# Kernel tuning notes

Hardware: AMD Instinct MI355X
Metric: run time of the kernel (lower is better)

Reference implementation:

```python
import jax, jax.numpy as jnp
import numpy as np

KS = 5          # kernel_size per pseudo-dim
DIM = 2         # pseudo-coordinate dims
KTOT = KS ** DIM  # 25 spline kernel slots
N_NODES = 50000
N_EDGES = 1600000
N_GRAPHS = 64
F_IN, H1, H2, N_CLS = 32, 32, 64, 10


def spline_basis(edge_attr):
    """Open B-spline basis, degree 1, dim=2, kernel_size=5.
    Returns basis [E,4] and flat kernel indices [E,4]."""
    v = edge_attr * (KS - 1)                    # [E,2] in [0, KS-1]
    lo = jnp.floor(v)
    frac = v - lo                               # [E,2]
    lo_i = lo.astype(jnp.int32)
    # per-dim basis values for offsets s in {0,1}: (1-frac), frac
    bas_d = jnp.stack([1.0 - frac, frac], axis=-1)            # [E,2,2]
    idx_d = jnp.minimum(lo_i[..., None] + jnp.arange(2, dtype=jnp.int32), KS - 1)  # [E,2,2]
    basis = bas_d[:, 0, :, None] * bas_d[:, 1, None, :]       # [E,2,2]
    kidx = idx_d[:, 0, :, None] + KS * idx_d[:, 1, None, :]   # [E,2,2]
    E = edge_attr.shape[0]
    return basis.reshape(E, 4), kidx.reshape(E, 4)


def spline_conv(x, src, dst, basis, kidx, W, Wroot, b):
    """SplineConv: gather x[src], spline-weight, scatter-mean to dst, + root + bias.
    W: [KTOT, Cin, Cout]."""
    N, Cin = x.shape
    x_j = x[src]                                # [E, Cin] gather
    # accumulate per-(node, kernel-slot) weighted sums; loop over 4 nonzero combos
    T = jnp.zeros((N * KTOT, Cin), dtype=x.dtype)
    for s in range(4):
        seg = dst * KTOT + kidx[:, s]
        T = T + jax.ops.segment_sum(basis[:, s, None] * x_j, seg,
                                    num_segments=N * KTOT)
    T = T.reshape(N, KTOT, Cin)
    out = jnp.einsum('nki,kio->no', T, W)       # [N, Cout]
    deg = jax.ops.segment_sum(jnp.ones_like(dst, dtype=x.dtype), dst,
                              num_segments=N)
    out = out / jnp.maximum(deg, 1.0)[:, None]  # aggr='mean'
    return out + x @ Wroot + b


def global_mean_pool(x, batch, num_graphs):
    s = jax.ops.segment_sum(x, batch, num_segments=num_graphs)
    cnt = jax.ops.segment_sum(jnp.ones((x.shape[0],), x.dtype), batch,
                              num_segments=num_graphs)
    return s / jnp.maximum(cnt, 1.0)[:, None]


def setup_inputs() -> dict:
    key = jax.random.key(0)
    ks = jax.random.split(key, 16)
    x = jax.random.normal(ks[0], (N_NODES, F_IN), jnp.float32)
    edge_index = jax.random.randint(ks[1], (2, N_EDGES), 0, N_NODES, jnp.int32)
    edge_attr = jax.random.uniform(ks[2], (N_EDGES, DIM), jnp.float32)
    batch = jnp.sort(jax.random.randint(ks[3], (N_NODES,), 0, N_GRAPHS, jnp.int32))

    def w(k, shape, fan_in):
        return jax.random.normal(k, shape, jnp.float32) / np.sqrt(fan_in)

    return {
        'x': x, 'edge_index': edge_index, 'edge_attr': edge_attr, 'batch': batch,
        'W1': w(ks[4], (KTOT, F_IN, H1), F_IN), 'root1': w(ks[5], (F_IN, H1), F_IN),
        'b1': jnp.zeros((H1,), jnp.float32),
        'W2': w(ks[6], (KTOT, H1, H2), H1), 'root2': w(ks[7], (H1, H2), H1),
        'b2': jnp.zeros((H2,), jnp.float32),
        'lin1_w': w(ks[8], (H2, 64), H2), 'lin1_b': jnp.zeros((64,), jnp.float32),
        'lin2_w': w(ks[9], (64, 64), 64), 'lin2_b': jnp.zeros((64,), jnp.float32),
        'lin3_w': w(ks[10], (64, N_CLS), 64), 'lin3_b': jnp.zeros((N_CLS,), jnp.float32),
    }


def reference(x, edge_index, edge_attr, batch, W1, root1, b1, W2, root2, b2,
              lin1_w, lin1_b, lin2_w, lin2_b, lin3_w, lin3_b):
    src, dst = edge_index[0], edge_index[1]
    basis, kidx = spline_basis(edge_attr)
    h = jax.nn.relu(spline_conv(x, src, dst, basis, kidx, W1, root1, b1))
    h = jax.nn.relu(spline_conv(h, src, dst, basis, kidx, W2, root2, b2))
    g = global_mean_pool(h, batch, N_GRAPHS)                # [B, 64]
    g = g * jax.nn.sigmoid(g @ lin1_w + lin1_b)
    g = g * jax.nn.sigmoid(g @ lin2_w + lin2_b)
    return jax.nn.log_softmax(g @ lin3_w + lin3_b, axis=1)  # [B, N_CLS]
```

## Files before the change

kernel.cpp:

```cpp
#include <hip/hip_runtime.h>
#include <hip/hip_bf16.h>
#include <hip/hip_fp16.h>
#include <cstdint>


typedef _Float16 half8 __attribute__((ext_vector_type(8)));
typedef float f32x4 __attribute__((ext_vector_type(4)));

__device__ __forceinline__ int lowb(const int* __restrict__ a, int n, int v) {
  int lo = 0, hi = n;
  while (lo < hi) { int m = (lo + hi) >> 1; if (a[m] < v) lo = m + 1; else hi = m; }
  return lo;
}

__global__ void hist_kernel(const int* __restrict__ dst, int E, int* __restrict__ deg) {
  int e = blockIdx.x * 256 + threadIdx.x;
  if (e < E) atomicAdd(&deg[dst[e]], 1);
}

__global__ __launch_bounds__(1024) void scan_block_kernel(
    const int* __restrict__ deg, int n, int* __restrict__ offs, int* __restrict__ bsums) {
  __shared__ int wsum[16];
  int t = threadIdx.x;
  int gi = blockIdx.x * 1024 + t;
  int v = (gi < n) ? deg[gi] : 0;
  int lane = t & 63, w = t >> 6;
  int x = v;
  #pragma unroll
  for (int d = 1; d < 64; d <<= 1) { int y = __shfl_up(x, d, 64); if (lane >= d) x += y; }
  if (lane == 63) wsum[w] = x;
  __syncthreads();
  if (w == 0) {
    int s = (lane < 16) ? wsum[lane] : 0;
    #pragma unroll
    for (int d = 1; d < 16; d <<= 1) { int y = __shfl_up(s, d, 64); if (lane >= d) s += y; }
    if (lane < 16) wsum[lane] = s;
  }
  __syncthreads();
  int add = (w > 0) ? wsum[w - 1] : 0;
  x += add;
  if (gi < n) offs[gi + 1] = x;
  if (t == 1023) bsums[blockIdx.x] = x;
}

__global__ __launch_bounds__(64) void scan_bsums_kernel(
    const int* __restrict__ bsums, int nb, int* __restrict__ boff) {
  int l = threadIdx.x;
  int v = (l < nb) ? bsums[l] : 0;
  int x = v;
  #pragma unroll
  for (int d = 1; d < 64; d <<= 1) { int y = __shfl_up(x, d, 64); if (l >= d) x += y; }
  if (l < nb) boff[l] = x - v;
}

__global__ void scan_add_kernel(int* __restrict__ offs, const int* __restrict__ boff, int n) {
  int i = blockIdx.x * 256 + threadIdx.x;
  if (i < n) offs[i + 1] += boff[i >> 10];
  if (i == 0) offs[0] = 0;
}

__global__ void scatter_kernel(const int* __restrict__ src, const int* __restrict__ dst,
                               const float2* __restrict__ attr, int E,
                               const int* __restrict__ offs, int* __restrict__ cursor,
                               int2* __restrict__ emeta) {
  int e = blockIdx.x * 256 + threadIdx.x;
  if (e < E) {
    float2 a = attr[e];
    float v0 = a.x * 4.f, v1 = a.y * 4.f;
    int i00 = min((int)v0, 3);
    int i10 = min((int)v1, 3);
    float f0 = v0 - (float)i00;
    float f1 = v1 - (float)i10;
    int f0q = (int)(f0 * 4095.f + 0.5f);
    int f1q = (int)(f1 * 4095.f + 0.5f);
    int yw = (i10 * 5 + i00) | (i10 << 5) | (f0q << 7) | (f1q << 19);
    int d = dst[e];
    int p = offs[d] + atomicAdd(&cursor[d], 1);
    emeta[p] = make_int2(src[e], yw);
  }
}

__global__ void x2h_kernel(const float* __restrict__ X, __half* __restrict__ Xh, int n) {
  int i = blockIdx.x * 256 + threadIdx.x;
  if (i < n) Xh[i] = __float2half(X[i]);
}

__global__ void w2h_kernel(const float* __restrict__ W, __half* __restrict__ Wh,
                           int ncolTot, int COUT) {
  int idx = blockIdx.x * 256 + threadIdx.x;
  if (idx < ncolTot * 32) {
    int col = idx >> 5, i = idx & 31;
    int kk = col / COUT, ch = col - kk * COUT;
    Wh[idx] = __float2half(W[(kk * 32 + i) * COUT + ch]);
  }
}

__global__ __launch_bounds__(256) void mfma_ygemm(
    const __half* __restrict__ Xh, const __half* __restrict__ Wh,
    __half* __restrict__ Y, int N, int ncol, int strideY) {
  __shared__ __half Ls[16 * 264];
  const int t = threadIdx.x;
  const int w = t >> 6, lane = t & 63;
  const int rowBase = blockIdx.x * 16;
  const int colBase = blockIdx.y * 256;
  const int kOff = (lane >> 4) * 8;
  int arow = min(rowBase + (lane & 15), N - 1);
  const half8 Af = *(const half8*)(Xh + (size_t)arow * 32 + kOff);
  half8 Bf[4];
  #pragma unroll
  for (int c = 0; c < 4; ++c) {
    int col = min(colBase + w * 64 + c * 16 + (lane & 15), ncol - 1);
    Bf[c] = *(const half8*)(Wh + (size_t)col * 32 + kOff);
  }
  f32x4 zero = {0.f, 0.f, 0.f, 0.f};
  f32x4 acc[4];
  #pragma unroll
  for (int c = 0; c < 4; ++c)
    acc[c] = __builtin_amdgcn_mfma_f32_16x16x32_f16(Af, Bf[c], zero, 0, 0, 0);
  #pragma unroll
  for (int c = 0; c < 4; ++c) {
    int col = w * 64 + c * 16 + (lane & 15);
    int r0 = (lane >> 4) * 4;
    #pragma unroll
    for (int r = 0; r < 4; ++r)
      Ls[(r0 + r) * 264 + col] = __float2half(acc[c][r]);
  }
  __syncthreads();
  int row = rowBase + (t >> 4);
  int cseg = (t & 15) * 16;
  if (row < N && colBase + cseg < ncol) {
    int4* dst = (int4*)(Y + (size_t)row * (size_t)strideY + colBase + cseg);
    const int4* srcp = (const int4*)(Ls + (t >> 4) * 264 + cseg);
    dst[0] = srcp[0];
    dst[1] = srcp[1];
  }
}

template <int COUT>
__global__ __launch_bounds__(256) void gather_kernel(
    const int2* __restrict__ emeta, const int* __restrict__ offs,
    const __half* __restrict__ Y, int strideY,
    float* __restrict__ hagg, int N, int g0, int g1, int first, int fused,
    const __half* __restrict__ X, const float* __restrict__ root,
    const float* __restrict__ bias, __half* __restrict__ hout) {
  __shared__ float Rs[32 * COUT];
  const int t = threadIdx.x;
  if (fused) {
    #pragma unroll
    for (int q = 0; q < (8 * COUT) / 256; ++q)
      *(float4*)&Rs[(t + q * 256) * 4] = *(const float4*)&root[(t + q * 256) * 4];
    __syncthreads();
  }
  const int w = t >> 6, lane = t & 63;
  const int n = blockIdx.x * 4 + w;
  if (n >= N) return;
  const int q4 = lane >> 4, r = lane & 15;
  const int di0 = q4 & 1, di1 = q4 >> 1;
  constexpr int CPL = COUT / 16;
  const int kBias = di0 + 5 * di1 - 5 * g0;
  const int laneCh = r * CPL;
  float acc[CPL];
  #pragma unroll
  for (int j = 0; j < CPL; ++j) acc[j] = 0.f;
  const int beg = offs[n], end = offs[n + 1];
  for (int b0 = beg; b0 < end; b0 += 64) {
    const int cnt = min(64, end - b0);
    int2 m = emeta[b0 + min(lane, cnt - 1)];
    int myS = m.x, myY = m.y;
    for (int j0 = 0; j0 < cnt; j0 += 4) {
      float wg[4];
      __half2 yv[4][CPL / 2];
      #pragma unroll
      for (int u = 0; u < 4; ++u) {
        int j = j0 + u;
        int jc = (j < cnt) ? j : 0;
        int s  = __builtin_amdgcn_readlane(myS, jc);
        int yw = __builtin_amdgcn_readlane(myY, jc);
        int k0 = yw & 31;
        int i10 = (yw >> 5) & 3;
        float f0 = (float)((yw >> 7) & 4095) * (1.f / 4095.f);
        float f1 = (float)((yw >> 19) & 4095) * (1.f / 4095.f);
        float wt = (di0 ? f0 : 1.f - f0) * (di1 ? f1 : 1.f - f1);
        bool skip = (j >= cnt) || (i10 < g0) || (i10 >= g1);
        wg[u] = skip ? 0.f : wt;
        int rowL = skip ? 0 : (k0 + kBias);
        const __half2* yp =
            (const __half2*)(Y + (size_t)s * (size_t)strideY + rowL * COUT + laneCh);
        #pragma unroll
        for (int p = 0; p < CPL / 2; ++p) yv[u][p] = yp[p];
      }
      #pragma unroll
      for (int u = 0; u < 4; ++u)
        #pragma unroll
        for (int p = 0; p < CPL / 2; ++p) {
          float2 f = __half22float2(yv[u][p]);
          acc[2 * p]     = fmaf(wg[u], f.x, acc[2 * p]);
          acc[2 * p + 1] = fmaf(wg[u], f.y, acc[2 * p + 1]);
        }
    }
  }
  #pragma unroll
  for (int j = 0; j < CPL; ++j) {
    acc[j] += __shfl_xor(acc[j], 16);
    acc[j] += __shfl_xor(acc[j], 32);
  }
  if (lane < 16) {
    if (!fused) {
      float* hp = hagg + (size_t)n * COUT + laneCh;
      if constexpr (CPL == 2) {
        float2 o = make_float2(acc[0], acc[1]);
        if (!first) { float2 p = *(float2*)hp; o.x += p.x; o.y += p.y; }
        *(float2*)hp = o;
      } else {
        float4 o = make_float4(acc[0], acc[1], acc[2], acc[3]);
        if (!first) {
          float4 p = *(float4*)hp;
          o.x += p.x; o.y += p.y; o.z += p.z; o.w += p.w;
        }
        *(float4*)hp = o;
      }
    } else {
      float rd = 1.f / (float)max(end - beg, 1);
      float a[CPL];
      #pragma unroll
      for (int j = 0; j < CPL; ++j) a[j] = acc[j] * rd;
      const __half* xr = X + (size_t)n * 32;
      for (int i = 0; i < 32; ++i) {
        float xv = __half2float(xr[i]);
        #pragma unroll
        for (int j = 0; j < CPL; ++j)
          a[j] = fmaf(xv, Rs[i * COUT + laneCh + j], a[j]);
      }
      #pragma unroll
      for (int j = 0; j < CPL; ++j) a[j] = fmaxf(a[j] + bias[laneCh + j], 0.f);
      __half2* op = (__half2*)(hout + (size_t)n * COUT + laneCh);
      #pragma unroll
      for (int p = 0; p < CPL / 2; ++p)
        op[p] = __floats2half2_rn(a[2 * p], a[2 * p + 1]);
    }
  }
}

template <int COUT>
__global__ __launch_bounds__(256) void finalize_kernel(
    const float* __restrict__ hagg, const __half* __restrict__ X,
    const float* __restrict__ root, const float* __restrict__ bias,
    const int* __restrict__ deg, __half* __restrict__ hout, int N) {
  __shared__ float Rs[32 * COUT];
  int t = threadIdx.x;
  #pragma unroll
  for (int q = 0; q < (32 * COUT) / 1024; ++q)
    *(float4*)&Rs[(q * 256 + t) * 4] = *(const float4*)&root[(q * 256 + t) * 4];
  __syncthreads();
  constexpr int TPN = COUT / 4;
  int gid = blockIdx.x * 256 + t;
  int n = gid / TPN;
  int c0 = (gid % TPN) * 4;
  if (n >= N) return;
  const __half* xr = X + (size_t)n * 32;
  float rd = 1.f / (float)max(deg[n], 1);
  float4 hv = *(const float4*)&hagg[(size_t)n * COUT + c0];
  float a0 = hv.x * rd, a1 = hv.y * rd, a2 = hv.z * rd, a3 = hv.w * rd;
  #pragma unroll
  for (int i = 0; i < 32; ++i) {
    float xv = __half2float(xr[i]);
    const float* rr = &Rs[i * COUT + c0];
    a0 = fmaf(xv, rr[0], a0);
    a1 = fmaf(xv, rr[1], a1);
    a2 = fmaf(xv, rr[2], a2);
    a3 = fmaf(xv, rr[3], a3);
  }
  __half2* op = (__half2*)(hout + (size_t)n * COUT + c0);
  op[0] = __floats2half2_rn(fmaxf(a0 + bias[c0 + 0], 0.f),
                            fmaxf(a1 + bias[c0 + 1], 0.f));
  op[1] = __floats2half2_rn(fmaxf(a2 + bias[c0 + 2], 0.f),
                            fmaxf(a3 + bias[c0 + 3], 0.f));
}

__global__ __launch_bounds__(256) void pool_kernel(
    const __half* __restrict__ h2, const int* __restrict__ batch, int N,
    float* __restrict__ poolacc) {
  __shared__ float red[4][64];
  int g = blockIdx.x >> 2, part = blockIdx.x & 3;
  int lo = lowb(batch, N, g), hi = lowb(batch, N, g + 1);
  int len = hi - lo;
  int b0 = lo + (int)(((long long)len * part) / 4);
  int b1 = lo + (int)(((long long)len * (part + 1)) / 4);
  int r = threadIdx.x >> 6, o = threadIdx.x & 63;
  float s = 0.f;
  for (int row = b0 + r; row < b1; row += 4)
    s += __half2float(h2[(size_t)row * 64 + o]);
  red[r][o] = s;
  __syncthreads();
  if (r == 0) {
    float v = red[0][o] + red[1][o] + red[2][o] + red[3][o];
    atomicAdd(&poolacc[g * 64 + o], v);
  }
}

__global__ __launch_bounds__(64) void head_kernel(
    const float* __restrict__ poolacc, const int* __restrict__ batch, int N,
    const float* __restrict__ w1, const float* __restrict__ b1,
    const float* __restrict__ w2, const float* __restrict__ b2,
    const float* __restrict__ w3, const float* __restrict__ b3,
    float* __restrict__ out) {
  __shared__ float gb[64];
  __shared__ float lg[10];
  int g = blockIdx.x, o = threadIdx.x;
  int lo = lowb(batch, N, g), hi = lowb(batch, N, g + 1);
  float cnt = fmaxf((float)(hi - lo), 1.f);
  float gv = poolacc[g * 64 + o] / cnt;
  gb[o] = gv;
  __syncthreads();
  float tacc = b1[o];
  for (int i = 0; i < 64; ++i) tacc = fmaf(gb[i], w1[i * 64 + o], tacc);
  gv = gv * (1.f / (1.f + expf(-tacc)));
  __syncthreads(); gb[o] = gv; __syncthreads();
  tacc = b2[o];
  for (int i = 0; i < 64; ++i) tacc = fmaf(gb[i], w2[i * 64 + o], tacc);
  gv = gv * (1.f / (1.f + expf(-tacc)));
  __syncthreads(); gb[o] = gv; __syncthreads();
  if (o < 10) {
    float l = b3[o];
    for (int i = 0; i < 64; ++i) l = fmaf(gb[i], w3[i * 10 + o], l);
    lg[o] = l;
  }
  __syncthreads();
  if (o < 10) {
    float m = lg[0];
    #pragma unroll
    for (int c = 1; c < 10; ++c) m = fmaxf(m, lg[c]);
    float s = 0.f;
    #pragma unroll
    for (int c = 0; c < 10; ++c) s += expf(lg[c] - m);
    out[g * 10 + o] = lg[o] - m - logf(s);
  }
}

extern "C" void kernel_launch(void* const* d_in, const int* in_sizes, int n_in,
                              void* d_out, int out_size, void* d_ws, size_t ws_size,
                              hipStream_t stream) {
  const float* x     = (const float*)d_in[0];
  const int*   ei    = (const int*)d_in[1];
  const float* eattr = (const float*)d_in[2];
  const int*   batch = (const int*)d_in[3];
  const float* W1    = (const float*)d_in[4];
  const float* root1 = (const float*)d_in[5];
  const float* b1    = (const float*)d_in[6];
  const float* W2    = (const float*)d_in[7];
  const float* root2 = (const float*)d_in[8];
  const float* b2    = (const float*)d_in[9];
  const float* l1w   = (const float*)d_in[10];
  const float* l1b   = (const float*)d_in[11];
  const float* l2w   = (const float*)d_in[12];
  const float* l2b   = (const float*)d_in[13];
  const float* l3w   = (const float*)d_in[14];
  const float* l3b   = (const float*)d_in[15];
  float* out = (float*)d_out;

  const int N = in_sizes[0] / 32;
  const int E = in_sizes[1] / 2;
  const int Npad = (N + 63) & ~63;

  char* base = (char*)d_ws;
  size_t off = 0;
  auto walloc = [&](size_t bytes) -> void* {
    off = (off + 255) & ~(size_t)255;
    void* p = base + off;
    off += bytes;
    return p;
  };
  int*    deg     = (int*)walloc((size_t)Npad * 4);
  int*    offs    = (int*)walloc((size_t)(N + 1) * 4);
  int*    cursor  = (int*)walloc((size_t)N * 4);
  int*    bsums   = (int*)walloc(64 * 4);
  int*    boff    = (int*)walloc(64 * 4);
  float*  poolacc = (float*)walloc(64 * 64 * 4);
  __half* h1h     = (__half*)walloc((size_t)N * 32 * 2);
  __half* h2h     = (__half*)walloc((size_t)N * 64 * 2);
  __half* Xh      = (__half*)walloc((size_t)N * 32 * 2);
  __half* Wh1     = (__half*)walloc((size_t)800 * 32 * 2);
  __half* Wh2     = (__half*)walloc((size_t)1600 * 32 * 2);
  float*  hagg    = (float*)walloc((size_t)N * 64 * 4);
  int2*   emeta   = (int2*)walloc((size_t)E * 8);
  off = (off + 255) & ~(size_t)255;
  size_t avail = (ws_size > off) ? (ws_size - off) : 0;
  __half* Yb = (__half*)(base + off);

  auto pickG = [&](int cout) -> int {
    size_t g5 = (size_t)N * 5 * cout * 2;
    if (avail < 2 * g5) return 0;
    size_t G = avail / g5 - 1;
    return (int)(G > 4 ? 4 : G);
  };
  int G1 = pickG(32), G2 = pickG(64);
  if (!G1 || !G2) return;

  const int* srcA = ei;
  const int* dstA = ei + E;

  hipMemsetAsync(deg, 0, (size_t)Npad * 4, stream);
  hipMemsetAsync(cursor, 0, (size_t)N * 4, stream);
  hipMemsetAsync(poolacc, 0, 64 * 64 * 4, stream);

  hist_kernel<<<(E + 255) / 256, 256, 0, stream>>>(dstA, E, deg);
  int nb = (N + 1023) / 1024;
  scan_block_kernel<<<nb, 1024, 0, stream>>>(deg, N, offs, bsums);
  scan_bsums_kernel<<<1, 64, 0, stream>>>(bsums, nb, boff);
  scan_add_kernel<<<(N + 255) / 256, 256, 0, stream>>>(offs, boff, N);
  scatter_kernel<<<(E + 255) / 256, 256, 0, stream>>>(srcA, dstA, (const float2*)eattr,
                                                      E, offs, cursor, emeta);
  x2h_kernel<<<((size_t)N * 32 + 255) / 256, 256, 0, stream>>>(x, Xh, N * 32);
  w2h_kernel<<<(800 * 32 + 255) / 256, 256, 0, stream>>>(W1, Wh1, 800, 32);
  w2h_kernel<<<(1600 * 32 + 255) / 256, 256, 0, stream>>>(W2, Wh2, 1600, 64);

  const int rowTiles = (N + 15) / 16;
  const int ggrid = (N + 3) / 4;
  for (int layer = 0; layer < 2; ++layer) {
    const __half* XinH = layer ? h1h : Xh;
    const __half* WhL  = layer ? Wh2 : Wh1;
    const float* rl    = layer ? root2 : root1;
    const float* bl    = layer ? b2 : b1;
    __half* HoutH      = layer ? h2h : h1h;
    const int G        = layer ? G2 : G1;
    const int COUT     = layer ? 64 : 32;
    const int fused    = (G >= 4) ? 1 : 0;
    for (int g0 = 0; g0 < 4; g0 += G) {
      int g1 = min(4, g0 + G);
      int kFirst = g0 * 5, kCount = (g1 - g0 + 1) * 5;
      int ncol = kCount * COUT;
      int first = (g0 == 0) ? 1 : 0;
      dim3 yg(rowTiles, (ncol + 255) / 256);
      mfma_ygemm<<<yg, 256, 0, stream>>>(XinH, WhL + (size_t)(kFirst * COUT) * 32,
                                         Yb, N, ncol, ncol);
      if (layer == 0)
        gather_kernel<32><<<ggrid, 256, 0, stream>>>(
            emeta, offs, Yb, ncol, hagg, N, g0, g1, first, fused,
            XinH, rl, bl, HoutH);
      else
        gather_kernel<64><<<ggrid, 256, 0, stream>>>(
            emeta, offs, Yb, ncol, hagg, N, g0, g1, first, fused,
            XinH, rl, bl, HoutH);
    }
    if (!fused) {
      if (layer == 0)
        finalize_kernel<32><<<((size_t)N * 8 + 255) / 256, 256, 0, stream>>>(
            hagg, XinH, rl, bl, deg, HoutH, N);
      else
        finalize_kernel<64><<<((size_t)N * 16 + 255) / 256, 256, 0, stream>>>(
            hagg, XinH, rl, bl, deg, HoutH, N);
    }
  }
  pool_kernel<<<256, 256, 0, stream>>>(h2h, batch, N, poolacc);
  head_kernel<<<64, 64, 0, stream>>>(poolacc, batch, N,
                                     l1w, l1b, l2w, l2b, l3w, l3b, out);
}
```

Measured before the change: 500.2 us.

## Precompute fp16 spline weights per edge and ballot-skip out-of-group edges in gather

The scatter kernel now stores the four bilinear basis weights per edge as packed fp16 pairs, plus a precomputed slot field, in a 16-byte record instead of an 8-byte quantized record. The gather kernel precomputes per-edge byte offsets and uses a wave ballot to iterate only over edges whose kernel row falls in the current group, skipping masked edges instead of issuing zero-weight loads. This removes per-edge dequantization ALU work and wasted Y loads across group passes. In exchange it doubles emeta memory traffic and drops the 4-way unrolled load batching, which can reduce memory-level parallelism. Byte offsets are computed in 32-bit int, which could overflow for large Y buffers.

```diff
diff --git a/kernel.cpp b/kernel.cpp
--- a/kernel.cpp
+++ b/kernel.cpp
@@ -6,6 +6,13 @@
 
 typedef _Float16 half8 __attribute__((ext_vector_type(8)));
 typedef float f32x4 __attribute__((ext_vector_type(4)));
+
+__device__ __forceinline__ int h2_as_int(__half2 h) {
+  int v; __builtin_memcpy(&v, &h, 4); return v;
+}
+__device__ __forceinline__ __half2 int_as_h2(int v) {
+  __half2 h; __builtin_memcpy(&h, &v, 4); return h;
+}
 
 __device__ __forceinline__ int lowb(const int* __restrict__ a, int n, int v) {
   int lo = 0, hi = n;
@@ -62,7 +69,7 @@
 __global__ void scatter_kernel(const int* __restrict__ src, const int* __restrict__ dst,
                                const float2* __restrict__ attr, int E,
                                const int* __restrict__ offs, int* __restrict__ cursor,
-                               int2* __restrict__ emeta) {
+                               int4* __restrict__ emeta) {
   int e = blockIdx.x * 256 + threadIdx.x;
   if (e < E) {
     float2 a = attr[e];
@@ -71,12 +78,15 @@
     int i10 = min((int)v1, 3);
     float f0 = v0 - (float)i00;
     float f1 = v1 - (float)i10;
-    int f0q = (int)(f0 * 4095.f + 0.5f);
-    int f1q = (int)(f1 * 4095.f + 0.5f);
-    int yw = (i10 * 5 + i00) | (i10 << 5) | (f0q << 7) | (f1q << 19);
+    float w00 = (1.f - f0) * (1.f - f1);
+    float w10 = f0 * (1.f - f1);
+    float w01 = (1.f - f0) * f1;
+    float w11 = f0 * f1;
     int d = dst[e];
     int p = offs[d] + atomicAdd(&cursor[d], 1);
-    emeta[p] = make_int2(src[e], yw);
+    emeta[p] = make_int4(src[e], (i10 * 5 + i00) | (i10 << 5),
+                         h2_as_int(__floats2half2_rn(w00, w10)),
+                         h2_as_int(__floats2half2_rn(w01, w11)));
   }
 }
 
@@ -138,7 +148,7 @@
 
 template <int COUT>
 __global__ __launch_bounds__(256) void gather_kernel(
-    const int2* __restrict__ emeta, const int* __restrict__ offs,
+    const int4* __restrict__ emeta, const int* __restrict__ offs,
     const __half* __restrict__ Y, int strideY,
     float* __restrict__ hagg, int N, int g0, int g1, int first, int fused,
     const __half* __restrict__ X, const float* __restrict__ root,
@@ -157,46 +167,41 @@
   const int q4 = lane >> 4, r = lane & 15;
   const int di0 = q4 & 1, di1 = q4 >> 1;
   constexpr int CPL = COUT / 16;
-  const int kBias = di0 + 5 * di1 - 5 * g0;
-  const int laneCh = r * CPL;
+  const int laneByte = (di1 * 5 * COUT + di0 * COUT + r * CPL) * 2;
+  const char* Ybase = (const char*)Y;
   float acc[CPL];
   #pragma unroll
   for (int j = 0; j < CPL; ++j) acc[j] = 0.f;
   const int beg = offs[n], end = offs[n + 1];
   for (int b0 = beg; b0 < end; b0 += 64) {
     const int cnt = min(64, end - b0);
-    int2 m = emeta[b0 + min(lane, cnt - 1)];
-    int myS = m.x, myY = m.y;
-    for (int j0 = 0; j0 < cnt; j0 += 4) {
-      float wg[4];
-      __half2 yv[4][CPL / 2];
-      #pragma unroll
-      for (int u = 0; u < 4; ++u) {
-        int j = j0 + u;
-        int jc = (j < cnt) ? j : 0;
-        int s  = __builtin_amdgcn_readlane(myS, jc);
-        int yw = __builtin_amdgcn_readlane(myY, jc);
-        int k0 = yw & 31;
-        int i10 = (yw >> 5) & 3;
-        float f0 = (float)((yw >> 7) & 4095) * (1.f / 4095.f);
-        float f1 = (float)((yw >> 19) & 4095) * (1.f / 4095.f);
-        float wt = (di0 ? f0 : 1.f - f0) * (di1 ? f1 : 1.f - f1);
-        bool skip = (j >= cnt) || (i10 < g0) || (i10 >= g1);
-        wg[u] = skip ? 0.f : wt;
-        int rowL = skip ? 0 : (k0 + kBias);
-        const __half2* yp =
-            (const __half2*)(Y + (size_t)s * (size_t)strideY + rowL * COUT + laneCh);
-        #pragma unroll
-        for (int p = 0; p < CPL / 2; ++p) yv[u][p] = yp[p];
+    int4 m = emeta[b0 + min(lane, cnt - 1)];
+    const int i10 = m.y >> 5;
+    const bool valid = (lane < cnt) & (i10 >= g0) & (i10 < g1);
+    int myByte = (m.x * strideY + ((m.y & 31) - g0 * 5) * COUT) * 2;
+    int myP0 = m.z, myP1 = m.w;
+    unsigned long long mask = __ballot(valid);
+    while (mask) {
+      int j = (int)__builtin_ctzll(mask);
+      mask &= mask - 1;
+      int b  = __builtin_amdgcn_readlane(myByte, j);
+      int p0 = __builtin_amdgcn_readlane(myP0, j);
+      int p1 = __builtin_amdgcn_readlane(myP1, j);
+      __half2 wp = int_as_h2(di1 ? p1 : p0);
+      float wq = __half2float(di0 ? __high2half(wp) : __low2half(wp));
+      const __half* yp = (const __half*)(Ybase + (size_t)(unsigned)(b + laneByte));
+      if constexpr (CPL == 2) {
+        __half2 yv = *(const __half2*)yp;
+        acc[0] = fmaf(wq, __half2float(__low2half(yv)), acc[0]);
+        acc[1] = fmaf(wq, __half2float(__high2half(yv)), acc[1]);
+      } else {
+        __half2 ya = *(const __half2*)yp;
+        __half2 yb = *(const __half2*)(yp + 2);
+        acc[0] = fmaf(wq, __half2float(__low2half(ya)), acc[0]);
+        acc[1] = fmaf(wq, __half2float(__high2half(ya)), acc[1]);
+        acc[2] = fmaf(wq, __half2float(__low2half(yb)), acc[2]);
+        acc[3] = fmaf(wq, __half2float(__high2half(yb)), acc[3]);
       }
-      #pragma unroll
-      for (int u = 0; u < 4; ++u)
-        #pragma unroll
-        for (int p = 0; p < CPL / 2; ++p) {
-          float2 f = __half22float2(yv[u][p]);
-          acc[2 * p]     = fmaf(wg[u], f.x, acc[2 * p]);
-          acc[2 * p + 1] = fmaf(wg[u], f.y, acc[2 * p + 1]);
-        }
     }
   }
   #pragma unroll
@@ -204,6 +209,7 @@
     acc[j] += __shfl_xor(acc[j], 16);
     acc[j] += __shfl_xor(acc[j], 32);
   }
+  const int laneCh = r * CPL;
   if (lane < 16) {
     if (!fused) {
       float* hp = hagg + (size_t)n * COUT + laneCh;
@@ -382,7 +388,7 @@
   __half* Wh1     = (__half*)walloc((size_t)800 * 32 * 2);
   __half* Wh2     = (__half*)walloc((size_t)1600 * 32 * 2);
   float*  hagg    = (float*)walloc((size_t)N * 64 * 4);
-  int2*   emeta   = (int2*)walloc((size_t)E * 8);
+  int4*   emeta   = (int4*)walloc((size_t)E * 16);
   off = (off + 255) & ~(size_t)255;
   size_t avail = (ws_size > off) ? (ws_size - off) : 0;
   __half* Yb = (__half*)(base + off);
```

New measurement: 521.7 us. +4.3%, slower.
